# Kernel tuning notes

Measured on AMD Instinct MI355X. Metric: run time of the kernel, lower is better.

Reference implementation:

```python
import jax, jax.numpy as jnp
import numpy as np

K_WRITE = 4
NUM_SLOTS = 16
VOCAB = 50257
D = 512


def layer_norm(x, g, b, eps=1e-5):
    mu = jnp.mean(x, axis=-1, keepdims=True)
    var = jnp.mean((x - mu) ** 2, axis=-1, keepdims=True)
    return (x - mu) * jax.lax.rsqrt(var + eps) * g + b


def setup_inputs() -> dict:
    key = jax.random.key(0)
    ks = jax.random.split(key, 16)
    B, T = 32, 2048
    s = lambda *sh: 1.0 / np.sqrt(sh[0])
    seq = jax.random.randint(ks[0], (B, T), 0, VOCAB)
    embed = jax.random.normal(ks[1], (VOCAB, D), jnp.float32) * 0.02
    W1 = jax.random.normal(ks[2], (D, 2 * D), jnp.float32) * s(D)
    b1 = jnp.zeros((2 * D,), jnp.float32)
    W2 = jax.random.normal(ks[3], (2 * D, D), jnp.float32) * s(2 * D)
    b2 = jnp.zeros((D,), jnp.float32)
    ln_g = jnp.ones((D,), jnp.float32)
    ln_b = jnp.zeros((D,), jnp.float32)
    Wg = jax.random.normal(ks[4], (D, NUM_SLOTS), jnp.float32) * s(D)
    bg = jnp.zeros((NUM_SLOTS,), jnp.float32)
    Wr = jax.random.normal(ks[5], (D, D), jnp.float32) * s(D)
    br = jnp.zeros((D,), jnp.float32)
    Wo = jax.random.normal(ks[6], (D, VOCAB), jnp.float32) * s(D)
    bo = jnp.zeros((VOCAB,), jnp.float32)
    return dict(seq=seq, embed=embed, W1=W1, b1=b1, W2=W2, b2=b2, ln_g=ln_g,
                ln_b=ln_b, Wg=Wg, bg=bg, Wr=Wr, br=br, Wo=Wo, bo=bo)


def forward(seq, embed, W1, b1, W2, b2, ln_g, ln_b, Wg, bg, Wr, br, Wo, bo):
    # Encoder: embed -> FFN residual -> layernorm
    h = embed[seq]                                  # [B,T,D]
    ff = jax.nn.relu(h @ W1 + b1) @ W2 + b2
    hiddens = layer_norm(h + ff, ln_g, ln_b)        # [B,T,D]

    ctx_h = hiddens[:, :-1, :]                      # [B,T-1,D]
    B, Tm1, Dd = ctx_h.shape
    k_w = min(K_WRITE, Tm1)

    # write_to_memory: gate -> topk -> gather -> scatter into zero memory
    gate_scores = jnp.mean(ctx_h @ Wg + bg, axis=-1)          # [B,T-1]
    _, top_idx = jax.lax.top_k(gate_scores, k_w)              # [B,k_w]
    gathered = jnp.take_along_axis(ctx_h, top_idx[:, :, None], axis=1)  # [B,k_w,D]
    slot_idx = jnp.arange(k_w) % NUM_SLOTS                    # unique since k_w<=slots
    mem = jnp.zeros((B, NUM_SLOTS, Dd), ctx_h.dtype).at[:, slot_idx, :].set(gathered)

    # small attention read
    q = hiddens[:, -1, :] @ Wr + br                 # [B,D]
    scores = jnp.einsum('bsd,bd->bs', mem, q)       # [B,slots]
    attn = jax.nn.softmax(scores, axis=-1)
    ctx = jnp.einsum('bs,bsd->bd', attn, mem)       # [B,D]
    return ctx @ Wo + bo                            # [B,vocab]


def reference(seq, embed, W1, b1, W2, b2, ln_g, ln_b, Wg, bg, Wr, br, Wo, bo):
    return forward(seq, embed, W1, b1, W2, b2, ln_g, ln_b, Wg, bg, Wr, br, Wo, bo)
```

## Files before the change

### kernel.cpp

```cpp
#include <hip/hip_runtime.h>
#include <stdint.h>

typedef __attribute__((ext_vector_type(8))) short bf16x8;
typedef __attribute__((ext_vector_type(4))) float f32x4;
typedef unsigned short ushortT;

#define DEV static __device__ __forceinline__

DEV unsigned short f2bf(float x) {
  union { float f; unsigned u; } v; v.f = x;
  unsigned r = v.u + 0x7fffu + ((v.u >> 16) & 1u);
  return (unsigned short)(r >> 16);
}
DEV float bf2f(unsigned short b) {
  union { unsigned u; float f; } v; v.u = ((unsigned)b) << 16; return v.f;
}
DEV void gll16(const void* g, void* l) {
  __builtin_amdgcn_global_load_lds((const __attribute__((address_space(1))) void*)g,
                                   (__attribute__((address_space(3))) void*)l, 16, 0, 0);
}

#define VMW(n) asm volatile("s_waitcnt vmcnt(" #n ")" ::: "memory")
#define RAWBAR() __builtin_amdgcn_s_barrier()
#define SCHED0() __builtin_amdgcn_sched_barrier(0)

__global__ void kPrep(const float* __restrict__ W1, const float* __restrict__ W2,
                      const float* __restrict__ Wg, const float* __restrict__ ln_g,
                      ushortT* __restrict__ W1t, ushortT* __restrict__ W2t,
                      float* __restrict__ gw, float* __restrict__ wgm) {
  const size_t t = (size_t)blockIdx.x * 256 + threadIdx.x;
  if (t < 524288) {
    int n = (int)(t & 1023), k = (int)(t >> 10);
    W1t[(size_t)n * 512 + k] = f2bf(W1[(size_t)k * 1024 + n]);
  } else if (t < 1048576) {
    size_t u = t - 524288;
    int n = (int)(u & 511), k = (int)(u >> 9);
    W2t[(size_t)n * 1024 + k] = f2bf(W2[(size_t)k * 512 + n]);
  } else if (t < 1048576 + 512) {
    int c = (int)(t - 1048576);
    float s = 0.f;
    for (int j = 0; j < 16; ++j) s += Wg[c * 16 + j];
    float m = s * (1.0f / 16.0f);
    wgm[c] = m;
    gw[c] = ln_g[c] * m;
  }
}

__global__ void kPrep2(const float* __restrict__ gw, const float* __restrict__ wgm,
                       const float* __restrict__ ln_b, const float* __restrict__ bg,
                       float* __restrict__ consts) {
  const int tid = threadIdx.x;
  float a = gw[tid];
  float c = ln_b[tid] * wgm[tid];
  #pragma unroll
  for (int s = 1; s < 64; s <<= 1) { a += __shfl_xor(a, s); c += __shfl_xor(c, s); }
  __shared__ float red[8][2];
  const int wv = tid >> 6, ln = tid & 63;
  if (ln == 0) { red[wv][0] = a; red[wv][1] = c; }
  __syncthreads();
  if (tid == 0) {
    float Cg = 0, Cb0 = 0;
    for (int k = 0; k < 8; ++k) { Cg += red[k][0]; Cb0 += red[k][1]; }
    float bgm = 0;
    for (int j = 0; j < 16; ++j) bgm += bg[j];
    bgm *= (1.0f / 16.0f);
    consts[0] = Cg; consts[1] = Cb0 + bgm; consts[2] = bgm;
  }
}

__global__ void kEmbed(const int* __restrict__ seq, const float* __restrict__ embed,
                       ushortT* __restrict__ h) {
  const size_t t = (size_t)blockIdx.x * 256 + threadIdx.x;
  const size_t row = t >> 6;
  const int seg = (int)(t & 63) * 8;
  const int tok = seq[row];
  const float4* src = (const float4*)(embed + (size_t)tok * 512 + seg);
  float4 x = src[0], y = src[1];
  uint4 u;
  u.x = (unsigned)f2bf(x.x) | ((unsigned)f2bf(x.y) << 16);
  u.y = (unsigned)f2bf(x.z) | ((unsigned)f2bf(x.w) << 16);
  u.z = (unsigned)f2bf(y.x) | ((unsigned)f2bf(y.y) << 16);
  u.w = (unsigned)f2bf(y.z) | ((unsigned)f2bf(y.w) << 16);
  *(uint4*)(h + row * 512 + seg) = u;
}


__global__ __launch_bounds__(512, 2) void kG1p(const ushortT* __restrict__ h,
                                               const ushortT* __restrict__ W1t,
                                               const float* __restrict__ b1,
                                               ushortT* __restrict__ Y) {
  __shared__ __align__(16) ushortT SH[49152];
  ushortT* Asb = SH;
  ushortT* Bsb = SH + 24576;
  const int tid = threadIdx.x, w = tid >> 6, l = tid & 63;
  const int b = blockIdx.x, xcd = b & 7, loc = b >> 3;
  const int nt = loc & 3, mtl = loc >> 2;
  const size_t m0 = (size_t)(xcd * 16 + mtl) * 256;
  const int n0 = nt * 256;
  const int rl = l & 15, gq = l >> 4;
  f32x4 acc[4][8] = {};

  auto stage = [&](int buf, int k0) {
    #pragma unroll
    for (int q = 0; q < 2; ++q) {
      const int c = w * 2 + q;
      gll16(h + (m0 + c * 16 + rl) * 512 + k0 + gq * 8, &Asb[buf * 8192 + c * 512]);
      gll16(W1t + (size_t)(n0 + c * 16 + rl) * 512 + k0 + gq * 8, &Bsb[buf * 8192 + c * 512]);
    }
  };

  const int wr = w >> 1, wc = w & 1, l8 = l * 8;
  auto compute = [&](int buf) {
    bf16x8 a[4], bb[8];
    #pragma unroll
    for (int i = 0; i < 4; ++i)
      a[i] = *(const bf16x8*)&Asb[buf * 8192 + (wr * 4 + i) * 512 + l8];
    #pragma unroll
    for (int j = 0; j < 8; ++j)
      bb[j] = *(const bf16x8*)&Bsb[buf * 8192 + (wc * 8 + j) * 512 + l8];
    #pragma unroll
    for (int i = 0; i < 4; ++i)
      #pragma unroll
      for (int j = 0; j < 8; ++j)
        acc[i][j] = __builtin_amdgcn_mfma_f32_16x16x32_bf16(a[i], bb[j], acc[i][j], 0, 0, 0);
  };

  stage(0, 0); stage(1, 32); stage(2, 64);
  for (int t = 0; t < 13; ++t) {
    VMW(8); RAWBAR(); SCHED0();
    compute(t % 3);
    SCHED0(); RAWBAR();
    stage(t % 3, (t + 3) * 32);
  }
  VMW(8); RAWBAR(); SCHED0(); compute(1); SCHED0(); RAWBAR();
  VMW(4); RAWBAR(); SCHED0(); compute(2); SCHED0(); RAWBAR();
  VMW(0); RAWBAR(); SCHED0(); compute(0);

  float bv[8];
  #pragma unroll
  for (int j = 0; j < 8; ++j) bv[j] = b1[n0 + wc * 128 + j * 16 + rl];

  #pragma unroll
  for (int P = 0; P < 2; ++P) {
    __syncthreads();
    if ((wr >> 1) == P) {
      const int lrb = (wr & 1) * 64;
      #pragma unroll
      for (int i = 0; i < 4; ++i) {
        #pragma unroll
        for (int j = 0; j < 8; ++j) {
          const int cl = wc * 128 + j * 16 + rl;
          #pragma unroll
          for (int r = 0; r < 4; ++r) {
            const int lr = lrb + i * 16 + gq * 4 + r;
            float v = acc[i][j][r] + bv[j];
            v = v > 0.0f ? v : 0.0f;
            SH[lr * 266 + cl] = f2bf(v);
          }
        }
      }
    }
    __syncthreads();
    #pragma unroll
    for (int it = 0; it < 8; ++it) {
      const int row = it * 16 + (tid >> 5);
      const int c8 = (tid & 31) * 8;
      uint4 v = *(const uint4*)&SH[row * 266 + c8];
      *(uint4*)&Y[(m0 + P * 128 + row) * 1024 + n0 + c8] = v;
    }
  }
}

__global__ __launch_bounds__(512, 2) void kG2p(const ushortT* __restrict__ Yb,
                                               const ushortT* __restrict__ W2t,
                                               const ushortT* __restrict__ h,
                                               const float* __restrict__ b2,
                                               const float* __restrict__ gw,
                                               float* __restrict__ partS, int R0) {
  __shared__ __align__(16) ushortT As[3][256 * 32];
  __shared__ __align__(16) ushortT Bs[3][256 * 32];
  __shared__ float part[256][2][3];
  const int tid = threadIdx.x, w = tid >> 6, l = tid & 63;
  const int b = blockIdx.x, xcd = b & 7, loc = b >> 3;
  const int nt = loc & 1, mtl = loc >> 1;
  const size_t m0 = (size_t)(xcd * 16 + mtl) * 256;
  const int n0 = nt * 256;
  const int rl = l & 15, gq = l >> 4;
  f32x4 acc[4][8] = {};

  auto stage = [&](int buf, int k0) {
    #pragma unroll
    for (int q = 0; q < 2; ++q) {
      const int c = w * 2 + q;
      gll16(Yb + (m0 + c * 16 + rl) * 1024 + k0 + gq * 8, &As[buf][c * 512]);
      gll16(W2t + (size_t)(n0 + c * 16 + rl) * 1024 + k0 + gq * 8, &Bs[buf][c * 512]);
    }
  };

  const int wr = w >> 1, wc = w & 1, l8 = l * 8;
  auto compute = [&](int buf) {
    bf16x8 a[4], bb[8];
    #pragma unroll
    for (int i = 0; i < 4; ++i)
      a[i] = *(const bf16x8*)&As[buf][(wr * 4 + i) * 512 + l8];
    #pragma unroll
    for (int j = 0; j < 8; ++j)
      bb[j] = *(const bf16x8*)&Bs[buf][(wc * 8 + j) * 512 + l8];
    #pragma unroll
    for (int i = 0; i < 4; ++i)
      #pragma unroll
      for (int j = 0; j < 8; ++j)
        acc[i][j] = __builtin_amdgcn_mfma_f32_16x16x32_bf16(a[i], bb[j], acc[i][j], 0, 0, 0);
  };

  stage(0, 0); stage(1, 32); stage(2, 64);
  for (int t = 0; t < 29; ++t) {
    VMW(8); RAWBAR(); SCHED0();
    compute(t % 3);
    SCHED0(); RAWBAR();
    stage(t % 3, (t + 3) * 32);
  }
  VMW(8); RAWBAR(); SCHED0(); compute(2); SCHED0(); RAWBAR();
  VMW(4); RAWBAR(); SCHED0(); compute(0); SCHED0(); RAWBAR();
  VMW(0); RAWBAR(); SCHED0(); compute(1);

  #pragma unroll
  for (int i = 0; i < 4; ++i) {
    #pragma unroll
    for (int r = 0; r < 4; ++r) {
      const int rowl = wr * 64 + i * 16 + gq * 4 + r;
      const size_t grow = (size_t)R0 + m0 + rowl;
      float s1 = 0, s2 = 0, s3 = 0;
      #pragma unroll
      for (int j = 0; j < 8; ++j) {
        const int col = n0 + wc * 128 + j * 16 + rl;
        const float z = acc[i][j][r] + b2[col] + bf2f(h[grow * 512 + col]);
        s1 += z; s2 += z * z; s3 += z * gw[col];
      }
      #pragma unroll
      for (int s = 1; s < 16; s <<= 1) {
        s1 += __shfl_xor(s1, s);
        s2 += __shfl_xor(s2, s);
        s3 += __shfl_xor(s3, s);
      }
      if (rl == 0) { part[rowl][wc][0] = s1; part[rowl][wc][1] = s2; part[rowl][wc][2] = s3; }
    }
  }
  __syncthreads();
  if (tid < 256) {
    const size_t grow = (size_t)R0 + m0 + tid;
    const float S1 = part[tid][0][0] + part[tid][1][0];
    const float S2 = part[tid][0][1] + part[tid][1][1];
    const float S3 = part[tid][0][2] + part[tid][1][2];
    float* p = partS + grow * 8 + nt * 4;
    p[0] = S1; p[1] = S2; p[2] = S3;
  }
}

__global__ void kTop(const float* __restrict__ partS, const float* __restrict__ consts,
                     float* __restrict__ scores, int* __restrict__ cidx,
                     int* __restrict__ ccnt) {
  const int b = blockIdx.x, tid = threadIdx.x;
  const float Cg = consts[0], Cb = consts[1];
  float v0 = -1e30f, v1 = -1e30f, v2 = -1e30f, v3 = -1e30f;
  for (int i = tid; i < 2047; i += 256) {
    const size_t row = (size_t)b * 2048 + i;
    const float* p = partS + row * 8;
    const float S1 = p[0] + p[4];
    const float S2 = p[1] + p[5];
    const float S3 = p[2] + p[6];
    const float mu = S1 * (1.0f / 512.0f);
    const float var = S2 * (1.0f / 512.0f) - mu * mu;
    const float x = rsqrtf(var + 1e-5f) * (S3 - mu * Cg) + Cb;
    scores[row] = x;
    if (x > v3) {
      if (x > v0)      { v3 = v2; v2 = v1; v1 = v0; v0 = x; }
      else if (x > v1) { v3 = v2; v2 = v1; v1 = x; }
      else if (x > v2) { v3 = v2; v2 = x; }
      else             { v3 = x; }
    }
  }
  __shared__ float lv[256][4];
  lv[tid][0] = v0; lv[tid][1] = v1; lv[tid][2] = v2; lv[tid][3] = v3;
  __syncthreads();
  for (int s = 128; s > 0; s >>= 1) {
    if (tid < s) {
      float m[8] = { lv[tid][0], lv[tid][1], lv[tid][2], lv[tid][3],
                     lv[tid + s][0], lv[tid + s][1], lv[tid + s][2], lv[tid + s][3] };
      #pragma unroll
      for (int k = 0; k < 4; ++k) {
        int mx = k;
        #pragma unroll
        for (int j2 = k + 1; j2 < 8; ++j2) if (m[j2] > m[mx]) mx = j2;
        const float tv = m[k]; m[k] = m[mx]; m[mx] = tv;
        lv[tid][k] = m[k];
      }
    }
    __syncthreads();
  }
  __shared__ int cnt;
  __shared__ float thr;
  if (tid == 0) { thr = lv[0][3] - 0.03f; cnt = 0; }
  __syncthreads();
  const float th = thr;
  const float* sc = scores + (size_t)b * 2048;
  for (int i = tid; i < 2047; i += 256) {
    if (sc[i] >= th) {
      const int p = atomicAdd(&cnt, 1);
      if (p < 24) cidx[b * 24 + p] = i;
    }
  }
  __syncthreads();
  if (tid == 0) ccnt[b] = cnt < 24 ? cnt : 24;
}

__global__ void kCompact(const int* __restrict__ ccnt, const int* __restrict__ cidx,
                         int* __restrict__ offs, int* __restrict__ rowsb,
                         int* __restrict__ rowsl, int* __restrict__ plast,
                         int* __restrict__ nrp) {
  const int tid = threadIdx.x;
  if (tid >= 32) return;
  int off = 0, nc = 0;
  for (int k = 0; k < 32; ++k) { const int c = ccnt[k]; if (k < tid) off += c; nc += c; }
  offs[tid] = off;
  const int cnt = ccnt[tid];
  for (int j = 0; j < cnt; ++j) { rowsb[off + j] = tid; rowsl[off + j] = cidx[tid * 24 + j]; }
  rowsb[nc + tid] = tid; rowsl[nc + tid] = 2047; plast[tid] = nc + tid;
  if (tid == 0) { offs[32] = nc; nrp[0] = nc + 32; }
}

__global__ void kGather(const int* __restrict__ nrp, const int* __restrict__ rowsb,
                        const int* __restrict__ rowsl, const int* __restrict__ seq,
                        const float* __restrict__ embed, float* __restrict__ H2) {
  const int p = blockIdx.x;
  if (p >= nrp[0]) return;
  const int b = rowsb[p], lr = rowsl[p];
  const size_t gr = (size_t)b * 2048 + lr;
  const int tok = seq[gr];
  const float* src = embed + (size_t)tok * 512;
  float* dst = H2 + (size_t)p * 512;
  for (int c = threadIdx.x; c < 512; c += 128) dst[c] = src[c];
}

__global__ __launch_bounds__(256) void kR1(const int* __restrict__ nrp,
                                           const float* __restrict__ H2,
                                           const float* __restrict__ W1,
                                           const float* __restrict__ b1,
                                           float* __restrict__ Y2) {
  const int p = blockIdx.y;
  if (p >= nrp[0]) return;
  const int col = blockIdx.x * 256 + threadIdx.x;
  __shared__ float hrow[512];
  for (int c = threadIdx.x; c < 512; c += 256) hrow[c] = H2[(size_t)p * 512 + c];
  __syncthreads();
  float a0 = 0, a1 = 0, a2 = 0, a3 = 0;
  #pragma unroll 4
  for (int k = 0; k < 512; k += 4) {
    a0 = fmaf(hrow[k + 0], W1[(size_t)(k + 0) * 1024 + col], a0);
    a1 = fmaf(hrow[k + 1], W1[(size_t)(k + 1) * 1024 + col], a1);
    a2 = fmaf(hrow[k + 2], W1[(size_t)(k + 2) * 1024 + col], a2);
    a3 = fmaf(hrow[k + 3], W1[(size_t)(k + 3) * 1024 + col], a3);
  }
  const float v = a0 + a1 + a2 + a3 + b1[col];
  Y2[(size_t)p * 1024 + col] = v > 0.0f ? v : 0.0f;
}

__global__ __launch_bounds__(256) void kR2(const int* __restrict__ nrp,
                                           const float* __restrict__ Y2,
                                           const float* __restrict__ W2,
                                           const float* __restrict__ b2,
                                           float* __restrict__ F2) {
  const int p = blockIdx.y;
  if (p >= nrp[0]) return;
  const int col = blockIdx.x * 256 + threadIdx.x;
  __shared__ float yrow[1024];
  for (int c = threadIdx.x; c < 1024; c += 256) yrow[c] = Y2[(size_t)p * 1024 + c];
  __syncthreads();
  float a0 = 0, a1 = 0, a2 = 0, a3 = 0;
  #pragma unroll 4
  for (int k = 0; k < 1024; k += 4) {
    a0 = fmaf(yrow[k + 0], W2[(size_t)(k + 0) * 512 + col], a0);
    a1 = fmaf(yrow[k + 1], W2[(size_t)(k + 1) * 512 + col], a1);
    a2 = fmaf(yrow[k + 2], W2[(size_t)(k + 2) * 512 + col], a2);
    a3 = fmaf(yrow[k + 3], W2[(size_t)(k + 3) * 512 + col], a3);
  }
  F2[(size_t)p * 512 + col] = a0 + a1 + a2 + a3 + b2[col];
}

__global__ void kR3(const int* __restrict__ nrp, const float* __restrict__ H2,
                    const float* __restrict__ F2, const float* __restrict__ ln_g,
                    const float* __restrict__ ln_b, const float* __restrict__ wgm,
                    const float* __restrict__ consts, float* __restrict__ LNR,
                    float* __restrict__ cscore) {
  const int p = blockIdx.x;
  if (p >= nrp[0]) return;
  const int tid = threadIdx.x;
  const int c0 = tid, c1 = tid + 256;
  const float z0 = H2[(size_t)p * 512 + c0] + F2[(size_t)p * 512 + c0];
  const float z1 = H2[(size_t)p * 512 + c1] + F2[(size_t)p * 512 + c1];
  float s1 = z0 + z1, s2 = z0 * z0 + z1 * z1;
  #pragma unroll
  for (int s = 1; s < 64; s <<= 1) { s1 += __shfl_xor(s1, s); s2 += __shfl_xor(s2, s); }
  __shared__ float red[4][2];
  __shared__ float stats[2];
  const int wv = tid >> 6, ln = tid & 63;
  if (ln == 0) { red[wv][0] = s1; red[wv][1] = s2; }
  __syncthreads();
  if (tid == 0) {
    const float S1 = red[0][0] + red[1][0] + red[2][0] + red[3][0];
    const float S2 = red[0][1] + red[1][1] + red[2][1] + red[3][1];
    const float mu = S1 * (1.0f / 512.0f);
    const float var = S2 * (1.0f / 512.0f) - mu * mu;
    stats[0] = mu; stats[1] = rsqrtf(var + 1e-5f);
  }
  __syncthreads();
  const float mu = stats[0], rstd = stats[1];
  const float l0 = (z0 - mu) * rstd * ln_g[c0] + ln_b[c0];
  const float l1 = (z1 - mu) * rstd * ln_g[c1] + ln_b[c1];
  LNR[(size_t)p * 512 + c0] = l0;
  LNR[(size_t)p * 512 + c1] = l1;
  float sp = l0 * wgm[c0] + l1 * wgm[c1];
  #pragma unroll
  for (int s = 1; s < 64; s <<= 1) sp += __shfl_xor(sp, s);
  if (ln == 0) red[wv][0] = sp;
  __syncthreads();
  if (tid == 0) cscore[p] = red[0][0] + red[1][0] + red[2][0] + red[3][0] + consts[2];
}

__global__ void kSel(const int* __restrict__ ccnt, const int* __restrict__ offs,
                     const int* __restrict__ rowsl, const int* __restrict__ plast,
                     const float* __restrict__ cscore, const float* __restrict__ LNR,
                     const float* __restrict__ Wr, const float* __restrict__ br,
                     float* __restrict__ ctx) {
  const int b = blockIdx.x, tid = threadIdx.x;
  __shared__ int psel[4];
  __shared__ float lnl[512];
  __shared__ float qs[512];
  __shared__ float aw[4];
  __shared__ float red[4][4];
  if (tid == 0) {
    const int cnt = ccnt[b], off = offs[b];
    float scv[24]; int lr[24]; bool tk[24];
    for (int j = 0; j < cnt; ++j) { scv[j] = cscore[off + j]; lr[j] = rowsl[off + j]; tk[j] = false; }
    for (int k = 0; k < 4; ++k) {
      int best = -1;
      for (int j = 0; j < cnt; ++j) {
        if (tk[j]) continue;
        if (best < 0 || scv[j] > scv[best] || (scv[j] == scv[best] && lr[j] < lr[best])) best = j;
      }
      tk[best] = true;
      psel[k] = off + best;
    }
  }
  __syncthreads();
  const int pl = plast[b];
  for (int c = tid; c < 512; c += 256) lnl[c] = LNR[(size_t)pl * 512 + c];
  __syncthreads();
  #pragma unroll
  for (int cc = 0; cc < 2; ++cc) {
    const int col = tid + cc * 256;
    float s = br[col];
    for (int d = 0; d < 512; ++d) s = fmaf(lnl[d], Wr[(size_t)d * 512 + col], s);
    qs[col] = s;
  }
  __syncthreads();
  const int p0 = psel[0], p1 = psel[1], p2 = psel[2], p3 = psel[3];
  float ps[4] = {0, 0, 0, 0};
  for (int d = tid; d < 512; d += 256) {
    const float qv = qs[d];
    ps[0] = fmaf(qv, LNR[(size_t)p0 * 512 + d], ps[0]);
    ps[1] = fmaf(qv, LNR[(size_t)p1 * 512 + d], ps[1]);
    ps[2] = fmaf(qv, LNR[(size_t)p2 * 512 + d], ps[2]);
    ps[3] = fmaf(qv, LNR[(size_t)p3 * 512 + d], ps[3]);
  }
  #pragma unroll
  for (int s = 1; s < 64; s <<= 1) {
    ps[0] += __shfl_xor(ps[0], s); ps[1] += __shfl_xor(ps[1], s);
    ps[2] += __shfl_xor(ps[2], s); ps[3] += __shfl_xor(ps[3], s);
  }
  const int wv = tid >> 6, ln = tid & 63;
  if (ln == 0) { red[wv][0] = ps[0]; red[wv][1] = ps[1]; red[wv][2] = ps[2]; red[wv][3] = ps[3]; }
  __syncthreads();
  if (tid == 0) {
    const float s0 = red[0][0] + red[1][0] + red[2][0] + red[3][0];
    const float s1 = red[0][1] + red[1][1] + red[2][1] + red[3][1];
    const float s2 = red[0][2] + red[1][2] + red[2][2] + red[3][2];
    const float s3 = red[0][3] + red[1][3] + red[2][3] + red[3][3];
    const float m = fmaxf(fmaxf(fmaxf(s0, s1), fmaxf(s2, s3)), 0.0f);
    const float e0 = expf(s0 - m), e1 = expf(s1 - m), e2 = expf(s2 - m), e3 = expf(s3 - m);
    const float den = e0 + e1 + e2 + e3 + 12.0f * expf(-m);
    aw[0] = e0 / den; aw[1] = e1 / den; aw[2] = e2 / den; aw[3] = e3 / den;
  }
  __syncthreads();
  const float a0 = aw[0], a1 = aw[1], a2 = aw[2], a3 = aw[3];
  #pragma unroll
  for (int cc = 0; cc < 2; ++cc) {
    const int col = tid + cc * 256;
    const float v = a0 * LNR[(size_t)p0 * 512 + col] + a1 * LNR[(size_t)p1 * 512 + col]
                  + a2 * LNR[(size_t)p2 * 512 + col] + a3 * LNR[(size_t)p3 * 512 + col];
    ctx[(size_t)b * 512 + col] = v;
  }
}

__global__ __launch_bounds__(256) void kOutAcc(const float* __restrict__ ctx,
                                               const float* __restrict__ Wo,
                                               float* __restrict__ partial) {
  const int tid = threadIdx.x;
  const int rg = tid >> 6;
  int col = blockIdx.x * 64 + (tid & 63);
  const int d0 = blockIdx.y * 128;
  __shared__ float lctx[32][128];
  for (int i = tid; i < 32 * 128; i += 256) {
    const int b = i >> 7, dd = i & 127;
    lctx[b][dd] = ctx[(size_t)b * 512 + d0 + dd];
  }
  __syncthreads();
  const bool valid = col < 50257;
  if (!valid) col = 50256;
  float acc[8] = {};
  for (int d4 = 0; d4 < 128; d4 += 4) {
    const float w0 = Wo[(size_t)(d0 + d4 + 0) * 50257 + col];
    const float w1 = Wo[(size_t)(d0 + d4 + 1) * 50257 + col];
    const float w2 = Wo[(size_t)(d0 + d4 + 2) * 50257 + col];
    const float w3 = Wo[(size_t)(d0 + d4 + 3) * 50257 + col];
    #pragma unroll
    for (int j = 0; j < 8; ++j) {
      const float4 cc = *(const float4*)&lctx[rg * 8 + j][d4];
      acc[j] = fmaf(cc.x, w0, fmaf(cc.y, w1, fmaf(cc.z, w2, fmaf(cc.w, w3, acc[j]))));
    }
  }
  if (valid) {
    #pragma unroll
    for (int j = 0; j < 8; ++j)
      partial[((size_t)blockIdx.y * 32 + rg * 8 + j) * 50257 + col] = acc[j];
  }
}

__global__ __launch_bounds__(256) void kOutRed(const float* __restrict__ partial,
                                               const float* __restrict__ bo,
                                               float* __restrict__ out) {
  const size_t i = (size_t)blockIdx.x * 256 + threadIdx.x;
  if (i >= (size_t)32 * 50257) return;
  const int col = (int)(i % 50257);
  float s = bo[col];
  #pragma unroll
  for (int q = 0; q < 4; ++q) s += partial[(size_t)q * 32 * 50257 + i];
  out[i] = s;
}

extern "C" void kernel_launch(void* const* d_in, const int* in_sizes, int n_in,
                              void* d_out, int out_size, void* d_ws, size_t ws_size,
                              hipStream_t stream) {
  const int*   seq   = (const int*)  d_in[0];
  const float* embed = (const float*)d_in[1];
  const float* W1    = (const float*)d_in[2];
  const float* b1    = (const float*)d_in[3];
  const float* W2    = (const float*)d_in[4];
  const float* b2    = (const float*)d_in[5];
  const float* ln_g  = (const float*)d_in[6];
  const float* ln_b  = (const float*)d_in[7];
  const float* Wg    = (const float*)d_in[8];
  const float* bg    = (const float*)d_in[9];
  const float* Wr    = (const float*)d_in[10];
  const float* br    = (const float*)d_in[11];
  const float* Wo    = (const float*)d_in[12];
  const float* bo    = (const float*)d_in[13];
  float* out = (float*)d_out;
  char* ws = (char*)d_ws;

  ushortT* W1t   = (ushortT*)(ws + 0);
  ushortT* W2t   = (ushortT*)(ws + 1048576);
  float* gw      = (float*)(ws + 2097152);
  float* wgm     = (float*)(ws + 2099200);
  float* consts  = (float*)(ws + 2101248);
  ushortT* h     = (ushortT*)(ws + 2101504);
  ushortT* Ybuf  = (ushortT*)(ws + 69210368);
  float* partial = (float*)(ws + 69210368);
  float* scores  = (float*)(ws + 136319232);
  int* cidx      = (int*)(ws + 136581376);
  int* ccnt      = (int*)(ws + 136584448);
  int* offs      = (int*)(ws + 136584576);
  int* nrp       = (int*)(ws + 136584832);
  int* plast     = (int*)(ws + 136585088);
  int* rowsb     = (int*)(ws + 136585344);
  int* rowsl     = (int*)(ws + 136588672);
  float* partS   = (float*)(ws + 136592000);
  float* H2      = (float*)(ws + 136592000);
  float* Y2      = (float*)(ws + 138295936);
  float* F2      = (float*)(ws + 141703808);
  float* LNR     = (float*)(ws + 143407744);
  float* csc     = (float*)(ws + 145111680);
  float* ctxb    = (float*)(ws + 145115008);

  kPrep <<<4098, 256, 0, stream>>>(W1, W2, Wg, ln_g, W1t, W2t, gw, wgm);
  kPrep2<<<1, 512, 0, stream>>>(gw, wgm, ln_b, bg, consts);
  kEmbed<<<16384, 256, 0, stream>>>(seq, embed, h);
  for (int c = 0; c < 2; ++c) {
    kG1p<<<512, 512, 0, stream>>>(h + (size_t)c * 32768 * 512, W1t, b1, Ybuf);
    kG2p<<<256, 512, 0, stream>>>(Ybuf, W2t, h, b2, gw, partS, c * 32768);
  }
  kTop    <<<32, 256, 0, stream>>>(partS, consts, scores, cidx, ccnt);
  kCompact<<<1, 64, 0, stream>>>(ccnt, cidx, offs, rowsb, rowsl, plast, nrp);
  kGather <<<800, 128, 0, stream>>>(nrp, rowsb, rowsl, seq, embed, H2);
  kR1<<<dim3(4, 800), 256, 0, stream>>>(nrp, H2, W1, b1, Y2);
  kR2<<<dim3(2, 800), 256, 0, stream>>>(nrp, Y2, W2, b2, F2);
  kR3<<<800, 256, 0, stream>>>(nrp, H2, F2, ln_g, ln_b, wgm, consts, LNR, csc);
  kSel<<<32, 256, 0, stream>>>(ccnt, offs, rowsl, plast, csc, LNR, Wr, br, ctxb);
  kOutAcc<<<dim3(786, 4), 256, 0, stream>>>(ctxb, Wo, partial);
  kOutRed<<<(32 * 50257 + 255) / 256, 256, 0, stream>>>(partial, bo, out);
}
```

Before: 443.6 us.

## Use bf16 MFMA for output projection and double-buffer G1 LDS pipeline

The output projection ctx@Wo moves from scalar FMA accumulation over four K-splits to a 32x32x16 bf16 MFMA kernel with two K-splits. Wo is converted to bf16 on the fly and ctx is written in bf16 by kSel. The first FFN GEMM drops from triple to double buffering to cut shared memory from 96KB to 64KB, which may allow more residency but gives less latency hiding. The MFMA path adds bf16 rounding error on the output logits.

```diff
diff --git a/kernel.cpp b/kernel.cpp
--- a/kernel.cpp
+++ b/kernel.cpp
@@ -3,6 +3,7 @@
 
 typedef __attribute__((ext_vector_type(8))) short bf16x8;
 typedef __attribute__((ext_vector_type(4))) float f32x4;
+typedef __attribute__((ext_vector_type(16))) float f32x16;
 typedef unsigned short ushortT;
 
 #define DEV static __device__ __forceinline__
@@ -84,14 +85,11 @@
   *(uint4*)(h + row * 512 + seg) = u;
 }
 
-
 __global__ __launch_bounds__(512, 2) void kG1p(const ushortT* __restrict__ h,
                                                const ushortT* __restrict__ W1t,
                                                const float* __restrict__ b1,
                                                ushortT* __restrict__ Y) {
-  __shared__ __align__(16) ushortT SH[49152];
-  ushortT* Asb = SH;
-  ushortT* Bsb = SH + 24576;
+  __shared__ __align__(16) ushortT SH[32768];
   const int tid = threadIdx.x, w = tid >> 6, l = tid & 63;
   const int b = blockIdx.x, xcd = b & 7, loc = b >> 3;
   const int nt = loc & 3, mtl = loc >> 2;
@@ -104,8 +102,8 @@
     #pragma unroll
     for (int q = 0; q < 2; ++q) {
       const int c = w * 2 + q;
-      gll16(h + (m0 + c * 16 + rl) * 512 + k0 + gq * 8, &Asb[buf * 8192 + c * 512]);
-      gll16(W1t + (size_t)(n0 + c * 16 + rl) * 512 + k0 + gq * 8, &Bsb[buf * 8192 + c * 512]);
+      gll16(h + (m0 + c * 16 + rl) * 512 + k0 + gq * 8, &SH[buf * 8192 + c * 512]);
+      gll16(W1t + (size_t)(n0 + c * 16 + rl) * 512 + k0 + gq * 8, &SH[16384 + buf * 8192 + c * 512]);
     }
   };
 
@@ -114,10 +112,10 @@
     bf16x8 a[4], bb[8];
     #pragma unroll
     for (int i = 0; i < 4; ++i)
-      a[i] = *(const bf16x8*)&Asb[buf * 8192 + (wr * 4 + i) * 512 + l8];
+      a[i] = *(const bf16x8*)&SH[buf * 8192 + (wr * 4 + i) * 512 + l8];
     #pragma unroll
     for (int j = 0; j < 8; ++j)
-      bb[j] = *(const bf16x8*)&Bsb[buf * 8192 + (wc * 8 + j) * 512 + l8];
+      bb[j] = *(const bf16x8*)&SH[16384 + buf * 8192 + (wc * 8 + j) * 512 + l8];
     #pragma unroll
     for (int i = 0; i < 4; ++i)
       #pragma unroll
@@ -125,26 +123,24 @@
         acc[i][j] = __builtin_amdgcn_mfma_f32_16x16x32_bf16(a[i], bb[j], acc[i][j], 0, 0, 0);
   };
 
-  stage(0, 0); stage(1, 32); stage(2, 64);
-  for (int t = 0; t < 13; ++t) {
-    VMW(8); RAWBAR(); SCHED0();
-    compute(t % 3);
+  stage(0, 0); stage(1, 32);
+  for (int t = 0; t < 14; ++t) {
+    VMW(4); RAWBAR(); SCHED0();
+    compute(t & 1);
     SCHED0(); RAWBAR();
-    stage(t % 3, (t + 3) * 32);
-  }
-  VMW(8); RAWBAR(); SCHED0(); compute(1); SCHED0(); RAWBAR();
-  VMW(4); RAWBAR(); SCHED0(); compute(2); SCHED0(); RAWBAR();
-  VMW(0); RAWBAR(); SCHED0(); compute(0);
+    stage(t & 1, (t + 2) * 32);
+  }
+  VMW(4); RAWBAR(); SCHED0(); compute(0); SCHED0(); RAWBAR();
+  VMW(0); RAWBAR(); SCHED0(); compute(1);
 
   float bv[8];
   #pragma unroll
   for (int j = 0; j < 8; ++j) bv[j] = b1[n0 + wc * 128 + j * 16 + rl];
 
   #pragma unroll
-  for (int P = 0; P < 2; ++P) {
+  for (int P = 0; P < 4; ++P) {
     __syncthreads();
-    if ((wr >> 1) == P) {
-      const int lrb = (wr & 1) * 64;
+    if (wr == P) {
       #pragma unroll
       for (int i = 0; i < 4; ++i) {
         #pragma unroll
@@ -152,7 +148,7 @@
           const int cl = wc * 128 + j * 16 + rl;
           #pragma unroll
           for (int r = 0; r < 4; ++r) {
-            const int lr = lrb + i * 16 + gq * 4 + r;
+            const int lr = i * 16 + gq * 4 + r;
             float v = acc[i][j][r] + bv[j];
             v = v > 0.0f ? v : 0.0f;
             SH[lr * 266 + cl] = f2bf(v);
@@ -162,11 +158,11 @@
     }
     __syncthreads();
     #pragma unroll
-    for (int it = 0; it < 8; ++it) {
+    for (int it = 0; it < 4; ++it) {
       const int row = it * 16 + (tid >> 5);
       const int c8 = (tid & 31) * 8;
       uint4 v = *(const uint4*)&SH[row * 266 + c8];
-      *(uint4*)&Y[(m0 + P * 128 + row) * 1024 + n0 + c8] = v;
+      *(uint4*)&Y[(m0 + P * 64 + row) * 1024 + n0 + c8] = v;
     }
   }
 }
@@ -431,7 +427,7 @@
                      const int* __restrict__ rowsl, const int* __restrict__ plast,
                      const float* __restrict__ cscore, const float* __restrict__ LNR,
                      const float* __restrict__ Wr, const float* __restrict__ br,
-                     float* __restrict__ ctx) {
+                     float* __restrict__ ctx, ushortT* __restrict__ ctxB) {
   const int b = blockIdx.x, tid = threadIdx.x;
   __shared__ int psel[4];
   __shared__ float lnl[512];
@@ -499,40 +495,42 @@
     const float v = a0 * LNR[(size_t)p0 * 512 + col] + a1 * LNR[(size_t)p1 * 512 + col]
                   + a2 * LNR[(size_t)p2 * 512 + col] + a3 * LNR[(size_t)p3 * 512 + col];
     ctx[(size_t)b * 512 + col] = v;
-  }
-}
-
-__global__ __launch_bounds__(256) void kOutAcc(const float* __restrict__ ctx,
-                                               const float* __restrict__ Wo,
-                                               float* __restrict__ partial) {
-  const int tid = threadIdx.x;
-  const int rg = tid >> 6;
-  int col = blockIdx.x * 64 + (tid & 63);
-  const int d0 = blockIdx.y * 128;
-  __shared__ float lctx[32][128];
-  for (int i = tid; i < 32 * 128; i += 256) {
-    const int b = i >> 7, dd = i & 127;
-    lctx[b][dd] = ctx[(size_t)b * 512 + d0 + dd];
-  }
-  __syncthreads();
-  const bool valid = col < 50257;
-  if (!valid) col = 50256;
-  float acc[8] = {};
-  for (int d4 = 0; d4 < 128; d4 += 4) {
-    const float w0 = Wo[(size_t)(d0 + d4 + 0) * 50257 + col];
-    const float w1 = Wo[(size_t)(d0 + d4 + 1) * 50257 + col];
-    const float w2 = Wo[(size_t)(d0 + d4 + 2) * 50257 + col];
-    const float w3 = Wo[(size_t)(d0 + d4 + 3) * 50257 + col];
-    #pragma unroll
-    for (int j = 0; j < 8; ++j) {
-      const float4 cc = *(const float4*)&lctx[rg * 8 + j][d4];
-      acc[j] = fmaf(cc.x, w0, fmaf(cc.y, w1, fmaf(cc.z, w2, fmaf(cc.w, w3, acc[j]))));
-    }
-  }
-  if (valid) {
-    #pragma unroll
-    for (int j = 0; j < 8; ++j)
-      partial[((size_t)blockIdx.y * 32 + rg * 8 + j) * 50257 + col] = acc[j];
+    ctxB[(size_t)b * 512 + col] = f2bf(v);
+  }
+}
+
+__global__ __launch_bounds__(512) void kOutM(const ushortT* __restrict__ ctxB,
+                                             const float* __restrict__ Wo,
+                                             float* __restrict__ partial) {
+  const int tid = threadIdx.x, w = tid >> 6, l = tid & 63;
+  const int ky = blockIdx.y;
+  int col = blockIdx.x * 256 + w * 32 + (l & 31);
+  const bool cv = col < 50257;
+  if (!cv) col = 50256;
+  const int kg = (l >> 5) * 8;
+  const int kb = ky * 256;
+  bf16x8 afr[16];
+  #pragma unroll
+  for (int ks = 0; ks < 16; ++ks)
+    afr[ks] = *(const bf16x8*)&ctxB[(size_t)(l & 31) * 512 + kb + ks * 16 + kg];
+  f32x16 acc = {};
+  #pragma unroll
+  for (int ks = 0; ks < 16; ++ks) {
+    const float* wp = Wo + (size_t)(kb + ks * 16 + kg) * 50257 + col;
+    float wv[8];
+    #pragma unroll
+    for (int j = 0; j < 8; ++j) wv[j] = wp[(size_t)j * 50257];
+    bf16x8 bfr;
+    #pragma unroll
+    for (int j = 0; j < 8; ++j) bfr[j] = (short)f2bf(wv[j]);
+    acc = __builtin_amdgcn_mfma_f32_32x32x16_bf16(afr[ks], bfr, acc, 0, 0, 0);
+  }
+  if (cv) {
+    #pragma unroll
+    for (int r = 0; r < 16; ++r) {
+      const int row = (r & 3) + 8 * (r >> 2) + 4 * (l >> 5);
+      partial[((size_t)ky * 32 + row) * 50257 + col] = acc[r];
+    }
   }
 }
 
@@ -544,7 +542,7 @@
   const int col = (int)(i % 50257);
   float s = bo[col];
   #pragma unroll
-  for (int q = 0; q < 4; ++q) s += partial[(size_t)q * 32 * 50257 + i];
+  for (int q = 0; q < 2; ++q) s += partial[(size_t)q * 32 * 50257 + i];
   out[i] = s;
 }
 
@@ -591,6 +589,7 @@
   float* LNR     = (float*)(ws + 143407744);
   float* csc     = (float*)(ws + 145111680);
   float* ctxb    = (float*)(ws + 145115008);
+  ushortT* ctxB  = (ushortT*)(ws + 145180544);
 
   kPrep <<<4098, 256, 0, stream>>>(W1, W2, Wg, ln_g, W1t, W2t, gw, wgm);
   kPrep2<<<1, 512, 0, stream>>>(gw, wgm, ln_b, bg, consts);
@@ -605,7 +604,7 @@
   kR1<<<dim3(4, 800), 256, 0, stream>>>(nrp, H2, W1, b1, Y2);
   kR2<<<dim3(2, 800), 256, 0, stream>>>(nrp, Y2, W2, b2, F2);
   kR3<<<800, 256, 0, stream>>>(nrp, H2, F2, ln_g, ln_b, wgm, consts, LNR, csc);
-  kSel<<<32, 256, 0, stream>>>(ccnt, offs, rowsl, plast, csc, LNR, Wr, br, ctxb);
-  kOutAcc<<<dim3(786, 4), 256, 0, stream>>>(ctxb, Wo, partial);
+  kSel<<<32, 256, 0, stream>>>(ccnt, offs, rowsl, plast, csc, LNR, Wr, br, ctxb, ctxB);
+  kOutM<<<dim3(197, 2), 512, 0, stream>>>(ctxB, Wo, partial);
   kOutRed<<<(32 * 50257 + 255) / 256, 256, 0, stream>>>(partial, bo, out);
 }
```

New measurement: 434.6 us. -2.0%, faster.
